# Optimization experiments

Hardware: AMD Instinct MI355X
Metric: run time of the kernel (lower is better)

The kernel has to match this reference:

```python
import jax, jax.numpy as jnp
import numpy as np

B, TD, TE, H, D, V = 64, 256, 256, 512, 256, 50000

def setup_inputs() -> dict:
    key = jax.random.key(0)
    ks = jax.random.split(key, 8)
    return {
        "enc_outputs": jax.random.normal(ks[0], (B, TE, H), jnp.float32),
        "dec_inputs": jax.random.randint(ks[1], (B, TD), 0, V, jnp.int32),
        "state_h": jax.random.normal(ks[2], (B, H), jnp.float32),
        "state_c": jax.random.normal(ks[3], (B, H), jnp.float32),
        "E": jax.random.normal(ks[4], (V, D), jnp.float32) * 0.02,
        "W": jax.random.normal(ks[5], (D, 4 * H), jnp.float32) * 0.02,
        "U": jax.random.normal(ks[6], (H, 4 * H), jnp.float32) * 0.02,
        "b": jnp.zeros((4 * H,), jnp.float32),
    }


def _masked_lstm(x, mask, h0, c0, W, U, b):
    """Keras-semantics masked LSTM: at masked steps states AND outputs are
    carried from the previous step. Gate order i, f, g(cell), o."""
    def step(carry, inp):
        h, c = carry
        xt, mt = inp  # xt: [B,D], mt: [B]
        z = xt @ W + h @ U + b  # [B,4H]
        i, f, g, o = jnp.split(z, 4, axis=-1)
        c_new = jax.nn.sigmoid(f) * c + jax.nn.sigmoid(i) * jnp.tanh(g)
        h_new = jax.nn.sigmoid(o) * jnp.tanh(c_new)
        m = mt[:, None]
        h2 = jnp.where(m, h_new, h)
        c2 = jnp.where(m, c_new, c)
        return (h2, c2), h2
    xs = (jnp.swapaxes(x, 0, 1), jnp.swapaxes(mask, 0, 1))  # time-major
    (hT, cT), hs = jax.lax.scan(step, (h0, c0), xs)
    return jnp.swapaxes(hs, 0, 1), hT, cT  # [B,Td,H]


def reference(enc_outputs, dec_inputs, state_h, state_c, E, W, U, b):
    mask = dec_inputs != 0  # mask_zero=True on Embedding
    x = E[dec_inputs]  # [B,Td,D]
    dec_outputs, hT, cT = _masked_lstm(x, mask, state_h, state_c, W, U, b)
    # Keras Attention (Luong dot, no scale): query=dec_outputs, key=value=enc_outputs
    scores = jnp.einsum('bqh,bkh->bqk', dec_outputs, enc_outputs)
    probs = jax.nn.softmax(scores, axis=-1)
    ctx = jnp.einsum('bqk,bkh->bqh', probs, enc_outputs)
    # query mask propagated from embedding zeroes masked query rows
    ctx = jnp.where(mask[..., None], ctx, 0.0)
    return (ctx, hT, cT)
```

## Files before the change

### kernel.cpp

```cpp
#include <hip/hip_runtime.h>
#include <stdint.h>

typedef __attribute__((ext_vector_type(4))) float f32x4;
typedef __attribute__((ext_vector_type(4))) int i32x4;
typedef __attribute__((ext_vector_type(4))) unsigned short u16x4;
typedef __attribute__((ext_vector_type(8))) __bf16 bf16x8;

#define NB 64
#define TD 256
#define TE 256
#define HH 512
#define DD 256
#define FH 2048
#define KT 768
#define LDK 776

#define WS_ENC   0u
#define WS_ENCT  16777216u
#define WS_DEC   33554432u
#define WS_HPING 50331648u
#define WS_FLAGS 50462720u
#define WS_WT    50528256u

#define OUT_HT 8388608u
#define OUT_CT 8421376u

__device__ inline unsigned short f2b(float f) {
  union { float f; unsigned u; } x; x.f = f;
  unsigned r = x.u + 0x7FFFu + ((x.u >> 16) & 1u);
  return (unsigned short)(r >> 16);
}
__device__ inline float sigm(float x)   { return 1.0f / (1.0f + __expf(-x)); }
__device__ inline float tanhf_(float x) { return 1.0f - 2.0f / (__expf(2.0f * x) + 1.0f); }

__device__ inline f32x4 mfma_bf16(i32x4 a, i32x4 b, f32x4 c) {
  return __builtin_amdgcn_mfma_f32_16x16x32_bf16(
      __builtin_bit_cast(bf16x8, a), __builtin_bit_cast(bf16x8, b), c, 0, 0, 0);
}

__device__ inline unsigned poll_flag(const unsigned* p) {
  unsigned v;
  asm volatile("global_load_dword %0, %1, off sc0 sc1\n\ts_waitcnt vmcnt(0)"
               : "=v"(v) : "v"(p) : "memory");
  return v;
}
__device__ inline void store_u16_wt(unsigned short* p, unsigned v) {
  asm volatile("global_store_short %0, %1, off sc0 sc1" :: "v"(p), "v"(v) : "memory");
}
__device__ inline void store_flag(unsigned* p, unsigned v) {
  asm volatile("s_waitcnt vmcnt(0)\n\tglobal_store_dword %0, %1, off sc0 sc1"
               :: "v"(p), "v"(v) : "memory");
}
__device__ inline void l2_inv() {
  asm volatile("s_waitcnt vmcnt(0)\n\tbuffer_inv sc1" ::: "memory");
}

__global__ __launch_bounds__(256) void enc_prep(const float* __restrict__ enc,
                                                unsigned short* __restrict__ enc_bf,
                                                unsigned short* __restrict__ encT_bf) {
  __shared__ float tile[64][65];
  const int bid = blockIdx.x;
  const int b  = bid >> 5;
  const int kt = (bid >> 3) & 3;
  const int ht = bid & 7;
  const int tr = threadIdx.x >> 6;
  const int tc = threadIdx.x & 63;
#pragma unroll
  for (int i = 0; i < 16; ++i) {
    const int ke = i * 4 + tr;
    const float v = enc[((size_t)b * TE + kt * 64 + ke) * HH + ht * 64 + tc];
    enc_bf[((size_t)b * TE + kt * 64 + ke) * HH + ht * 64 + tc] = f2b(v);
    tile[ke][tc] = v;
  }
  __syncthreads();
  const int hr4 = threadIdx.x >> 4;
  const int k4  = (threadIdx.x & 15) * 4;
#pragma unroll
  for (int jr = 0; jr < 4; ++jr) {
    const int hr = jr * 16 + hr4;
    u16x4 p = { f2b(tile[k4 + 0][hr]), f2b(tile[k4 + 1][hr]),
                f2b(tile[k4 + 2][hr]), f2b(tile[k4 + 3][hr]) };
    *(u16x4*)&encT_bf[((size_t)b * HH + ht * 64 + hr) * TE + kt * 64 + k4] = p;
  }
}

__global__ __launch_bounds__(256) void w_prep(const float* __restrict__ W,
                                              const float* __restrict__ U,
                                              unsigned short* __restrict__ wT) {
  __shared__ float tile[64][65];
  const int kt = blockIdx.x >> 5;
  const int ct = blockIdx.x & 31;
  const int tr = threadIdx.x >> 6;
  const int tc = threadIdx.x & 63;
#pragma unroll
  for (int i = 0; i < 16; ++i) {
    const int kr = i * 4 + tr;
    const int k  = kt * 64 + kr;
    const float v = (k < DD) ? W[(size_t)k * FH + ct * 64 + tc]
                             : U[(size_t)(k - DD) * FH + ct * 64 + tc];
    tile[kr][tc] = v;
  }
  __syncthreads();
  const int cr4 = threadIdx.x >> 4;
  const int k4  = (threadIdx.x & 15) * 4;
#pragma unroll
  for (int jr = 0; jr < 4; ++jr) {
    const int cr = jr * 16 + cr4;
    u16x4 p = { f2b(tile[k4 + 0][cr]), f2b(tile[k4 + 1][cr]),
                f2b(tile[k4 + 2][cr]), f2b(tile[k4 + 3][cr]) };
    *(u16x4*)&wT[((size_t)ct * 64 + cr) * KT + kt * 64 + k4] = p;
  }
}

__global__ __launch_bounds__(256) void h0_prep(const float* __restrict__ h0,
                                               unsigned short* __restrict__ h_ping,
                                               unsigned* __restrict__ flags) {
  const int i = blockIdx.x * 256 + threadIdx.x;
  if (i < NB * HH) h_ping[i] = f2b(h0[i]);
  if (i < 2 * TD * 32) flags[i] = 0u;
}

__global__ __launch_bounds__(64, 1) void lstm_kernel(
    const float* __restrict__ E, const int* __restrict__ ids,
    const float* __restrict__ h0f, const float* __restrict__ c0f,
    const unsigned short* __restrict__ wT, const float* __restrict__ bias,
    unsigned short* __restrict__ h_ping,
    unsigned short* __restrict__ dec_bf,
    float* __restrict__ out,
    unsigned* __restrict__ flags)
{
  const int lane = threadIdx.x;
  const int g  = blockIdx.x >> 5;
  const int s  = blockIdx.x & 31;
  const int u0 = s << 4;
  const int lhi = lane >> 4;
  const int llo = lane & 15;

  __shared__ __align__(16) unsigned short wt[64 * LDK];

  {
    const int r = lane;
    const int c = (r >> 4) * 512 + u0 + (r & 15);
    const unsigned short* src = wT + (size_t)c * KT;
#pragma unroll 8
    for (int j = 0; j < 96; ++j)
      *(i32x4*)&wt[r * LDK + j * 8] = *(const i32x4*)(src + j * 8);
  }
  __syncthreads();

  float bb[4];
#pragma unroll
  for (int gg = 0; gg < 4; ++gg) bb[gg] = bias[gg * 512 + u0 + llo];

  float h_reg[2][4], c_reg[2][4];
#pragma unroll
  for (int mt = 0; mt < 2; ++mt)
#pragma unroll
    for (int r = 0; r < 4; ++r) {
      const int b = g * 32 + mt * 16 + lhi * 4 + r;
      h_reg[mt][r] = h0f[b * HH + u0 + llo];
      c_reg[mt][r] = c0f[b * HH + u0 + llo];
    }

  unsigned short* hp0 = h_ping;
  unsigned short* hp1 = h_ping + NB * HH;

  for (int t = 0; t < TD; ++t) {
    const unsigned short* h_src = (t & 1) ? hp1 : hp0;
    unsigned short*       h_dst = (t & 1) ? hp0 : hp1;

    int xid[2], mid[2][4];
#pragma unroll
    for (int mt = 0; mt < 2; ++mt) {
      xid[mt] = ids[(g * 32 + mt * 16 + llo) * TD + t];
#pragma unroll
      for (int r = 0; r < 4; ++r)
        mid[mt][r] = ids[(g * 32 + mt * 16 + lhi * 4 + r) * TD + t];
    }

    i32x4 xf[2][8];
#pragma unroll
    for (int mt = 0; mt < 2; ++mt)
#pragma unroll
      for (int kk = 0; kk < 8; ++kk) {
        const float* ep = E + (size_t)xid[mt] * DD + kk * 32 + lhi * 8;
        f32x4 lo = *(const f32x4*)ep;
        f32x4 hi = *(const f32x4*)(ep + 4);
        union { i32x4 i; unsigned short sh[8]; } u;
        u.sh[0] = f2b(lo[0]); u.sh[1] = f2b(lo[1]); u.sh[2] = f2b(lo[2]); u.sh[3] = f2b(lo[3]);
        u.sh[4] = f2b(hi[0]); u.sh[5] = f2b(hi[1]); u.sh[6] = f2b(hi[2]); u.sh[7] = f2b(hi[3]);
        xf[mt][kk] = u.i;
      }

    f32x4 acc[2][4];
#pragma unroll
    for (int mt = 0; mt < 2; ++mt)
#pragma unroll
      for (int gg = 0; gg < 4; ++gg) acc[mt][gg] = (f32x4){0.f, 0.f, 0.f, 0.f};
#pragma unroll
    for (int kk = 0; kk < 8; ++kk) {
      const int ko = kk * 32 + lhi * 8;
#pragma unroll
      for (int gg = 0; gg < 4; ++gg) {
        i32x4 bfr = *(const i32x4*)&wt[(gg * 16 + llo) * LDK + ko];
        acc[0][gg] = mfma_bf16(xf[0][kk], bfr, acc[0][gg]);
        acc[1][gg] = mfma_bf16(xf[1][kk], bfr, acc[1][gg]);
      }
    }

    if (t > 0) {
      const unsigned* f = flags + ((size_t)g * TD + (t - 1)) * 32;
      for (;;) {
        unsigned v = (lane < 32) ? poll_flag(f + lane) : 1u;
        if (__all(v != 0)) break;
        __builtin_amdgcn_s_sleep(2);
      }
      l2_inv();
    }

    {
      const unsigned short* hb0 = h_src + (size_t)(g * 32 + llo) * HH + lhi * 8;
      const unsigned short* hb1 = hb0 + 16 * HH;
#pragma unroll
      for (int kk = 0; kk < 16; ++kk) {
        i32x4 a0 = *(const i32x4*)(hb0 + kk * 32);
        i32x4 a1 = *(const i32x4*)(hb1 + kk * 32);
        const int ko = DD + kk * 32 + lhi * 8;
#pragma unroll
        for (int gg = 0; gg < 4; ++gg) {
          i32x4 bfr = *(const i32x4*)&wt[(gg * 16 + llo) * LDK + ko];
          acc[0][gg] = mfma_bf16(a0, bfr, acc[0][gg]);
          acc[1][gg] = mfma_bf16(a1, bfr, acc[1][gg]);
        }
      }
    }

#pragma unroll
    for (int mt = 0; mt < 2; ++mt) {
#pragma unroll
      for (int r = 0; r < 4; ++r) {
        const float zi = acc[mt][0][r] + bb[0];
        const float zf = acc[mt][1][r] + bb[1];
        const float zg = acc[mt][2][r] + bb[2];
        const float zo = acc[mt][3][r] + bb[3];
        const float cn = sigm(zf) * c_reg[mt][r] + sigm(zi) * tanhf_(zg);
        const float hn = sigm(zo) * tanhf_(cn);
        if (mid[mt][r] != 0) { c_reg[mt][r] = cn; h_reg[mt][r] = hn; }
        const int b = g * 32 + mt * 16 + lhi * 4 + r;
        const unsigned hb = f2b(h_reg[mt][r]);
        store_u16_wt(h_dst + (size_t)b * HH + u0 + llo, hb);
        __builtin_nontemporal_store((unsigned short)hb,
            &dec_bf[((size_t)b * TD + t) * HH + u0 + llo]);
      }
    }

    if (t < TD - 1) {
      if (lane == 0)
        store_flag(flags + ((size_t)g * TD + t) * 32 + s, 1u);
      else
        asm volatile("s_waitcnt vmcnt(0)" ::: "memory");
    }
  }

#pragma unroll
  for (int mt = 0; mt < 2; ++mt)
#pragma unroll
    for (int r = 0; r < 4; ++r) {
      const int b = g * 32 + mt * 16 + lhi * 4 + r;
      out[OUT_HT + (size_t)b * HH + u0 + llo] = h_reg[mt][r];
      out[OUT_CT + (size_t)b * HH + u0 + llo] = c_reg[mt][r];
    }
}

__global__ __launch_bounds__(64, 1) void attn_kernel(
    const unsigned short* __restrict__ dec_bf,
    const unsigned short* __restrict__ enc_bf,
    const unsigned short* __restrict__ encT_bf,
    const int* __restrict__ ids,
    float* __restrict__ out)
{
  const int lane = threadIdx.x;
  const int b  = blockIdx.x >> 4;
  const int q0 = (blockIdx.x & 15) << 4;
  const int lhi = lane >> 4, llo = lane & 15;

  __shared__ __align__(16) unsigned short plds[16 * 264];

  i32x4 qf[16];
  const unsigned short* qb = dec_bf + ((size_t)b * TD + q0 + llo) * HH + lhi * 8;
#pragma unroll
  for (int kk = 0; kk < 16; ++kk) qf[kk] = *(const i32x4*)(qb + kk * 32);

  f32x4 sc[16];
#pragma unroll
  for (int ke = 0; ke < 16; ++ke) sc[ke] = (f32x4){0.f, 0.f, 0.f, 0.f};
#pragma unroll
  for (int kk = 0; kk < 16; ++kk) {
    const unsigned short* eb = enc_bf + ((size_t)b * TE + llo) * HH + kk * 32 + lhi * 8;
#pragma unroll
    for (int ke = 0; ke < 16; ++ke)
      sc[ke] = mfma_bf16(qf[kk], *(const i32x4*)(eb + (size_t)ke * 16 * HH), sc[ke]);
  }

  float mx[4], rinv[4];
#pragma unroll
  for (int r = 0; r < 4; ++r) {
    float m = sc[0][r];
#pragma unroll
    for (int ke = 1; ke < 16; ++ke) m = fmaxf(m, sc[ke][r]);
#pragma unroll
    for (int off = 1; off <= 8; off <<= 1) m = fmaxf(m, __shfl_xor(m, off));
    mx[r] = m;
  }
  float sm[4] = {0.f, 0.f, 0.f, 0.f};
#pragma unroll
  for (int ke = 0; ke < 16; ++ke)
#pragma unroll
    for (int r = 0; r < 4; ++r) {
      const float p = __expf(sc[ke][r] - mx[r]);
      sc[ke][r] = p;
      sm[r] += p;
    }
#pragma unroll
  for (int r = 0; r < 4; ++r) {
    float ss = sm[r];
#pragma unroll
    for (int off = 1; off <= 8; off <<= 1) ss += __shfl_xor(ss, off);
    rinv[r] = 1.0f / ss;
  }

#pragma unroll
  for (int ke = 0; ke < 16; ++ke)
#pragma unroll
    for (int r = 0; r < 4; ++r)
      plds[(lhi * 4 + r) * 264 + ke * 16 + llo] = f2b(sc[ke][r]);
  __syncthreads();

  int mq[4];
#pragma unroll
  for (int r = 0; r < 4; ++r) mq[r] = ids[b * TD + q0 + lhi * 4 + r];

  i32x4 pf[8];
#pragma unroll
  for (int k2 = 0; k2 < 8; ++k2)
    pf[k2] = *(const i32x4*)&plds[llo * 264 + k2 * 32 + lhi * 8];

#pragma unroll
  for (int hh = 0; hh < 2; ++hh) {
    f32x4 cacc[16];
#pragma unroll
    for (int hn = 0; hn < 16; ++hn) cacc[hn] = (f32x4){0.f, 0.f, 0.f, 0.f};
#pragma unroll
    for (int k2 = 0; k2 < 8; ++k2) {
      const unsigned short* tb = encT_bf + ((size_t)b * HH + hh * 256 + llo) * TE + k2 * 32 + lhi * 8;
#pragma unroll
      for (int hn = 0; hn < 16; ++hn)
        cacc[hn] = mfma_bf16(pf[k2], *(const i32x4*)(tb + (size_t)hn * 16 * TE), cacc[hn]);
    }
#pragma unroll
    for (int hn = 0; hn < 16; ++hn)
#pragma unroll
      for (int r = 0; r < 4; ++r) {
        const float vv = mq[r] ? cacc[hn][r] * rinv[r] : 0.0f;
        out[((size_t)b * TD + q0 + lhi * 4 + r) * HH + hh * 256 + hn * 16 + llo] = vv;
      }
  }
}

extern "C" void kernel_launch(void* const* d_in, const int* in_sizes, int n_in,
                              void* d_out, int out_size, void* d_ws, size_t ws_size,
                              hipStream_t stream) {
  const float* enc  = (const float*)d_in[0];
  const int*   ids  = (const int*)d_in[1];
  const float* h0   = (const float*)d_in[2];
  const float* c0   = (const float*)d_in[3];
  const float* E    = (const float*)d_in[4];
  const float* W    = (const float*)d_in[5];
  const float* U    = (const float*)d_in[6];
  const float* bias = (const float*)d_in[7];
  float* out = (float*)d_out;
  char* ws = (char*)d_ws;

  unsigned short* enc_bf  = (unsigned short*)(ws + WS_ENC);
  unsigned short* encT_bf = (unsigned short*)(ws + WS_ENCT);
  unsigned short* dec_bf  = (unsigned short*)(ws + WS_DEC);
  unsigned short* h_ping  = (unsigned short*)(ws + WS_HPING);
  unsigned*       flags   = (unsigned*)(ws + WS_FLAGS);
  unsigned short* wT      = (unsigned short*)(ws + WS_WT);

  enc_prep<<<2048, 256, 0, stream>>>(enc, enc_bf, encT_bf);
  w_prep<<<384, 256, 0, stream>>>(W, U, wT);
  h0_prep<<<128, 256, 0, stream>>>(h0, h_ping, flags);
  lstm_kernel<<<64, 64, 0, stream>>>(E, ids, h0, c0, wT, bias, h_ping, dec_bf, out, flags);
  attn_kernel<<<1024, 64, 0, stream>>>(dec_bf, enc_bf, encT_bf, ids, out);
}
```

Measured before the change: 2.253 ms.

## Tighten LSTM step handoff: bypass loads, drop L2 invalidate, stage ids in LDS

The per-step cross-block handoff is restructured. The buffer_inv L2 invalidate is removed, and the h vector is instead read with sc0 sc1 bypass loads, issued as one batch with a single drain before the MFMAs. The h stores and the flag store are now issued before the dec_bf output stores, so the flag waits only on the h stores, and the polling sleep is shortened. Token ids are also preloaded into LDS once per block, so per-step global id loads disappear. The change shortens the serial critical path of the recurrence, but it depends on the bypass loads being coherent without an invalidate and uses more registers and LDS.

```diff
diff --git a/kernel.cpp b/kernel.cpp
--- a/kernel.cpp
+++ b/kernel.cpp
@@ -44,15 +44,19 @@
                : "=v"(v) : "v"(p) : "memory");
   return v;
 }
+__device__ inline i32x4 load4_bypass(const void* p) {
+  i32x4 v;
+  asm volatile("global_load_dwordx4 %0, %1, off sc0 sc1" : "=v"(v) : "v"(p) : "memory");
+  return v;
+}
 __device__ inline void store_u16_wt(unsigned short* p, unsigned v) {
   asm volatile("global_store_short %0, %1, off sc0 sc1" :: "v"(p), "v"(v) : "memory");
 }
+__device__ inline void vm_drain() {
+  asm volatile("s_waitcnt vmcnt(0)" ::: "memory");
+}
 __device__ inline void store_flag(unsigned* p, unsigned v) {
-  asm volatile("s_waitcnt vmcnt(0)\n\tglobal_store_dword %0, %1, off sc0 sc1"
-               :: "v"(p), "v"(v) : "memory");
-}
-__device__ inline void l2_inv() {
-  asm volatile("s_waitcnt vmcnt(0)\n\tbuffer_inv sc1" ::: "memory");
+  asm volatile("global_store_dword %0, %1, off sc0 sc1" :: "v"(p), "v"(v) : "memory");
 }
 
 __global__ __launch_bounds__(256) void enc_prep(const float* __restrict__ enc,
@@ -137,6 +141,7 @@
   const int llo = lane & 15;
 
   __shared__ __align__(16) unsigned short wt[64 * LDK];
+  __shared__ int ids_l[32][260];
 
   {
     const int r = lane;
@@ -146,6 +151,10 @@
     for (int j = 0; j < 96; ++j)
       *(i32x4*)&wt[r * LDK + j * 8] = *(const i32x4*)(src + j * 8);
   }
+  for (int idx = lane; idx < 32 * 256; idx += 64) {
+    const int row = idx >> 8, tt = idx & 255;
+    ids_l[row][tt] = ids[(g * 32 + row) * TD + tt];
+  }
   __syncthreads();
 
   float bb[4];
@@ -172,10 +181,9 @@
     int xid[2], mid[2][4];
 #pragma unroll
     for (int mt = 0; mt < 2; ++mt) {
-      xid[mt] = ids[(g * 32 + mt * 16 + llo) * TD + t];
-#pragma unroll
-      for (int r = 0; r < 4; ++r)
-        mid[mt][r] = ids[(g * 32 + mt * 16 + lhi * 4 + r) * TD + t];
+      xid[mt] = ids_l[mt * 16 + llo][t];
+#pragma unroll
+      for (int r = 0; r < 4; ++r) mid[mt][r] = ids_l[mt * 16 + lhi * 4 + r][t];
     }
 
     i32x4 xf[2][8];
@@ -213,28 +221,34 @@
       for (;;) {
         unsigned v = (lane < 32) ? poll_flag(f + lane) : 1u;
         if (__all(v != 0)) break;
-        __builtin_amdgcn_s_sleep(2);
-      }
-      l2_inv();
+        __builtin_amdgcn_s_sleep(1);
+      }
     }
 
     {
       const unsigned short* hb0 = h_src + (size_t)(g * 32 + llo) * HH + lhi * 8;
       const unsigned short* hb1 = hb0 + 16 * HH;
+      i32x4 ha0[16], ha1[16];
 #pragma unroll
       for (int kk = 0; kk < 16; ++kk) {
-        i32x4 a0 = *(const i32x4*)(hb0 + kk * 32);
-        i32x4 a1 = *(const i32x4*)(hb1 + kk * 32);
+        ha0[kk] = load4_bypass(hb0 + kk * 32);
+        ha1[kk] = load4_bypass(hb1 + kk * 32);
+      }
+      vm_drain();
+      __builtin_amdgcn_sched_barrier(0);
+#pragma unroll
+      for (int kk = 0; kk < 16; ++kk) {
         const int ko = DD + kk * 32 + lhi * 8;
 #pragma unroll
         for (int gg = 0; gg < 4; ++gg) {
           i32x4 bfr = *(const i32x4*)&wt[(gg * 16 + llo) * LDK + ko];
-          acc[0][gg] = mfma_bf16(a0, bfr, acc[0][gg]);
-          acc[1][gg] = mfma_bf16(a1, bfr, acc[1][gg]);
+          acc[0][gg] = mfma_bf16(ha0[kk], bfr, acc[0][gg]);
+          acc[1][gg] = mfma_bf16(ha1[kk], bfr, acc[1][gg]);
         }
       }
     }
 
+    unsigned hb_out[2][4];
 #pragma unroll
     for (int mt = 0; mt < 2; ++mt) {
 #pragma unroll
@@ -246,20 +260,31 @@
         const float cn = sigm(zf) * c_reg[mt][r] + sigm(zi) * tanhf_(zg);
         const float hn = sigm(zo) * tanhf_(cn);
         if (mid[mt][r] != 0) { c_reg[mt][r] = cn; h_reg[mt][r] = hn; }
-        const int b = g * 32 + mt * 16 + lhi * 4 + r;
-        const unsigned hb = f2b(h_reg[mt][r]);
-        store_u16_wt(h_dst + (size_t)b * HH + u0 + llo, hb);
-        __builtin_nontemporal_store((unsigned short)hb,
-            &dec_bf[((size_t)b * TD + t) * HH + u0 + llo]);
+        hb_out[mt][r] = f2b(h_reg[mt][r]);
       }
     }
 
     if (t < TD - 1) {
+#pragma unroll
+      for (int mt = 0; mt < 2; ++mt)
+#pragma unroll
+        for (int r = 0; r < 4; ++r) {
+          const int b = g * 32 + mt * 16 + lhi * 4 + r;
+          store_u16_wt(h_dst + (size_t)b * HH + u0 + llo, hb_out[mt][r]);
+        }
+      vm_drain();
       if (lane == 0)
         store_flag(flags + ((size_t)g * TD + t) * 32 + s, 1u);
-      else
-        asm volatile("s_waitcnt vmcnt(0)" ::: "memory");
-    }
+    }
+
+#pragma unroll
+    for (int mt = 0; mt < 2; ++mt)
+#pragma unroll
+      for (int r = 0; r < 4; ++r) {
+        const int b = g * 32 + mt * 16 + lhi * 4 + r;
+        __builtin_nontemporal_store((unsigned short)hb_out[mt][r],
+            &dec_bf[((size_t)b * TD + t) * HH + u0 + llo]);
+      }
   }
 
 #pragma unroll
```

New measurement: 1.921 ms. 1.17x faster.

## Replace persistent flag-synchronized LSTM kernel with per-timestep kernel launches

Applied to the files above, without the earlier changes.

The persistent LSTM kernel, which used global-memory flags, polling and L2 invalidation to synchronize 64 blocks across timesteps, is replaced by one small kernel launch per timestep. Stream ordering now provides the inter-step barrier. The cell state lives in a global workspace buffer, and the weights are read from global memory (L2) on every step instead of being staged once in LDS. This trades the spin-wait cost for 256 kernel launch overheads plus repeated weight and state traffic. The final hT output now comes from the bf16-rounded h rather than the fp32 register value.

```diff
diff --git a/kernel.cpp b/kernel.cpp
--- a/kernel.cpp
+++ b/kernel.cpp
@@ -13,14 +13,13 @@
 #define DD 256
 #define FH 2048
 #define KT 768
-#define LDK 776
 
 #define WS_ENC   0u
 #define WS_ENCT  16777216u
 #define WS_DEC   33554432u
 #define WS_HPING 50331648u
-#define WS_FLAGS 50462720u
-#define WS_WT    50528256u
+#define WS_CST   50462720u
+#define WS_WT    50593792u
 
 #define OUT_HT 8388608u
 #define OUT_CT 8421376u
@@ -30,29 +29,16 @@
   unsigned r = x.u + 0x7FFFu + ((x.u >> 16) & 1u);
   return (unsigned short)(r >> 16);
 }
+__device__ inline float b2f(unsigned hs) {
+  union { unsigned u; float f; } x; x.u = hs << 16;
+  return x.f;
+}
 __device__ inline float sigm(float x)   { return 1.0f / (1.0f + __expf(-x)); }
 __device__ inline float tanhf_(float x) { return 1.0f - 2.0f / (__expf(2.0f * x) + 1.0f); }
 
 __device__ inline f32x4 mfma_bf16(i32x4 a, i32x4 b, f32x4 c) {
   return __builtin_amdgcn_mfma_f32_16x16x32_bf16(
       __builtin_bit_cast(bf16x8, a), __builtin_bit_cast(bf16x8, b), c, 0, 0, 0);
-}
-
-__device__ inline unsigned poll_flag(const unsigned* p) {
-  unsigned v;
-  asm volatile("global_load_dword %0, %1, off sc0 sc1\n\ts_waitcnt vmcnt(0)"
-               : "=v"(v) : "v"(p) : "memory");
-  return v;
-}
-__device__ inline void store_u16_wt(unsigned short* p, unsigned v) {
-  asm volatile("global_store_short %0, %1, off sc0 sc1" :: "v"(p), "v"(v) : "memory");
-}
-__device__ inline void store_flag(unsigned* p, unsigned v) {
-  asm volatile("s_waitcnt vmcnt(0)\n\tglobal_store_dword %0, %1, off sc0 sc1"
-               :: "v"(p), "v"(v) : "memory");
-}
-__device__ inline void l2_inv() {
-  asm volatile("s_waitcnt vmcnt(0)\n\tbuffer_inv sc1" ::: "memory");
 }
 
 __global__ __launch_bounds__(256) void enc_prep(const float* __restrict__ enc,
@@ -113,21 +99,24 @@
 }
 
 __global__ __launch_bounds__(256) void h0_prep(const float* __restrict__ h0,
+                                               const float* __restrict__ c0,
                                                unsigned short* __restrict__ h_ping,
-                                               unsigned* __restrict__ flags) {
+                                               float* __restrict__ c_st) {
   const int i = blockIdx.x * 256 + threadIdx.x;
-  if (i < NB * HH) h_ping[i] = f2b(h0[i]);
-  if (i < 2 * TD * 32) flags[i] = 0u;
-}
-
-__global__ __launch_bounds__(64, 1) void lstm_kernel(
+  if (i < NB * HH) {
+    h_ping[i] = f2b(h0[i]);
+    c_st[i] = c0[i];
+  }
+}
+
+__global__ __launch_bounds__(64, 1) void lstm_step(
     const float* __restrict__ E, const int* __restrict__ ids,
-    const float* __restrict__ h0f, const float* __restrict__ c0f,
     const unsigned short* __restrict__ wT, const float* __restrict__ bias,
-    unsigned short* __restrict__ h_ping,
+    float* __restrict__ c_st,
+    const unsigned short* __restrict__ h_src,
+    unsigned short* __restrict__ h_dst,
     unsigned short* __restrict__ dec_bf,
-    float* __restrict__ out,
-    unsigned* __restrict__ flags)
+    float* __restrict__ out, int t)
 {
   const int lane = threadIdx.x;
   const int g  = blockIdx.x >> 5;
@@ -136,140 +125,91 @@
   const int lhi = lane >> 4;
   const int llo = lane & 15;
 
-  __shared__ __align__(16) unsigned short wt[64 * LDK];
-
-  {
-    const int r = lane;
-    const int c = (r >> 4) * 512 + u0 + (r & 15);
-    const unsigned short* src = wT + (size_t)c * KT;
-#pragma unroll 8
-    for (int j = 0; j < 96; ++j)
-      *(i32x4*)&wt[r * LDK + j * 8] = *(const i32x4*)(src + j * 8);
-  }
-  __syncthreads();
-
-  float bb[4];
-#pragma unroll
-  for (int gg = 0; gg < 4; ++gg) bb[gg] = bias[gg * 512 + u0 + llo];
-
-  float h_reg[2][4], c_reg[2][4];
+  int xid[2], mid[2][4];
+#pragma unroll
+  for (int mt = 0; mt < 2; ++mt) {
+    xid[mt] = ids[(g * 32 + mt * 16 + llo) * TD + t];
+#pragma unroll
+    for (int r = 0; r < 4; ++r)
+      mid[mt][r] = ids[(g * 32 + mt * 16 + lhi * 4 + r) * TD + t];
+  }
+
+  i32x4 xf[2][8];
 #pragma unroll
   for (int mt = 0; mt < 2; ++mt)
+#pragma unroll
+    for (int kk = 0; kk < 8; ++kk) {
+      const float* ep = E + (size_t)xid[mt] * DD + kk * 32 + lhi * 8;
+      f32x4 lo = *(const f32x4*)ep;
+      f32x4 hi = *(const f32x4*)(ep + 4);
+      union { i32x4 i; unsigned short sh[8]; } u;
+      u.sh[0] = f2b(lo[0]); u.sh[1] = f2b(lo[1]); u.sh[2] = f2b(lo[2]); u.sh[3] = f2b(lo[3]);
+      u.sh[4] = f2b(hi[0]); u.sh[5] = f2b(hi[1]); u.sh[6] = f2b(hi[2]); u.sh[7] = f2b(hi[3]);
+      xf[mt][kk] = u.i;
+    }
+
+  const unsigned short* hb0 = h_src + (size_t)(g * 32 + llo) * HH + lhi * 8;
+  const unsigned short* hb1 = hb0 + 16 * HH;
+  i32x4 ha0[16], ha1[16];
+#pragma unroll
+  for (int kk = 0; kk < 16; ++kk) {
+    ha0[kk] = *(const i32x4*)(hb0 + kk * 32);
+    ha1[kk] = *(const i32x4*)(hb1 + kk * 32);
+  }
+
+  f32x4 acc[2][4];
+#pragma unroll
+  for (int mt = 0; mt < 2; ++mt)
+#pragma unroll
+    for (int gg = 0; gg < 4; ++gg) acc[mt][gg] = (f32x4){0.f, 0.f, 0.f, 0.f};
+
+#pragma unroll
+  for (int kk = 0; kk < 8; ++kk) {
+    const int ko = kk * 32 + lhi * 8;
+#pragma unroll
+    for (int gg = 0; gg < 4; ++gg) {
+      i32x4 bfr = *(const i32x4*)(wT + (size_t)(gg * 512 + u0 + llo) * KT + ko);
+      acc[0][gg] = mfma_bf16(xf[0][kk], bfr, acc[0][gg]);
+      acc[1][gg] = mfma_bf16(xf[1][kk], bfr, acc[1][gg]);
+    }
+  }
+#pragma unroll
+  for (int kk = 0; kk < 16; ++kk) {
+    const int ko = DD + kk * 32 + lhi * 8;
+#pragma unroll
+    for (int gg = 0; gg < 4; ++gg) {
+      i32x4 bfr = *(const i32x4*)(wT + (size_t)(gg * 512 + u0 + llo) * KT + ko);
+      acc[0][gg] = mfma_bf16(ha0[kk], bfr, acc[0][gg]);
+      acc[1][gg] = mfma_bf16(ha1[kk], bfr, acc[1][gg]);
+    }
+  }
+
+#pragma unroll
+  for (int mt = 0; mt < 2; ++mt) {
 #pragma unroll
     for (int r = 0; r < 4; ++r) {
       const int b = g * 32 + mt * 16 + lhi * 4 + r;
-      h_reg[mt][r] = h0f[b * HH + u0 + llo];
-      c_reg[mt][r] = c0f[b * HH + u0 + llo];
-    }
-
-  unsigned short* hp0 = h_ping;
-  unsigned short* hp1 = h_ping + NB * HH;
-
-  for (int t = 0; t < TD; ++t) {
-    const unsigned short* h_src = (t & 1) ? hp1 : hp0;
-    unsigned short*       h_dst = (t & 1) ? hp0 : hp1;
-
-    int xid[2], mid[2][4];
-#pragma unroll
-    for (int mt = 0; mt < 2; ++mt) {
-      xid[mt] = ids[(g * 32 + mt * 16 + llo) * TD + t];
-#pragma unroll
-      for (int r = 0; r < 4; ++r)
-        mid[mt][r] = ids[(g * 32 + mt * 16 + lhi * 4 + r) * TD + t];
-    }
-
-    i32x4 xf[2][8];
-#pragma unroll
-    for (int mt = 0; mt < 2; ++mt)
-#pragma unroll
-      for (int kk = 0; kk < 8; ++kk) {
-        const float* ep = E + (size_t)xid[mt] * DD + kk * 32 + lhi * 8;
-        f32x4 lo = *(const f32x4*)ep;
-        f32x4 hi = *(const f32x4*)(ep + 4);
-        union { i32x4 i; unsigned short sh[8]; } u;
-        u.sh[0] = f2b(lo[0]); u.sh[1] = f2b(lo[1]); u.sh[2] = f2b(lo[2]); u.sh[3] = f2b(lo[3]);
-        u.sh[4] = f2b(hi[0]); u.sh[5] = f2b(hi[1]); u.sh[6] = f2b(hi[2]); u.sh[7] = f2b(hi[3]);
-        xf[mt][kk] = u.i;
+      const size_t si = (size_t)b * HH + u0 + llo;
+      const float zi = acc[mt][0][r] + bias[0 * 512 + u0 + llo];
+      const float zf = acc[mt][1][r] + bias[1 * 512 + u0 + llo];
+      const float zg = acc[mt][2][r] + bias[2 * 512 + u0 + llo];
+      const float zo = acc[mt][3][r] + bias[3 * 512 + u0 + llo];
+      const float c_old = c_st[si];
+      const unsigned h_old = h_src[si];
+      const float cn = sigm(zf) * c_old + sigm(zi) * tanhf_(zg);
+      const float hn = sigm(zo) * tanhf_(cn);
+      const int m = mid[mt][r];
+      const float c_new = m ? cn : c_old;
+      const unsigned hb = m ? f2b(hn) : h_old;
+      c_st[si] = c_new;
+      h_dst[si] = (unsigned short)hb;
+      dec_bf[((size_t)b * TD + t) * HH + u0 + llo] = (unsigned short)hb;
+      if (t == TD - 1) {
+        out[OUT_HT + si] = b2f(hb);
+        out[OUT_CT + si] = c_new;
       }
-
-    f32x4 acc[2][4];
-#pragma unroll
-    for (int mt = 0; mt < 2; ++mt)
-#pragma unroll
-      for (int gg = 0; gg < 4; ++gg) acc[mt][gg] = (f32x4){0.f, 0.f, 0.f, 0.f};
-#pragma unroll
-    for (int kk = 0; kk < 8; ++kk) {
-      const int ko = kk * 32 + lhi * 8;
-#pragma unroll
-      for (int gg = 0; gg < 4; ++gg) {
-        i32x4 bfr = *(const i32x4*)&wt[(gg * 16 + llo) * LDK + ko];
-        acc[0][gg] = mfma_bf16(xf[0][kk], bfr, acc[0][gg]);
-        acc[1][gg] = mfma_bf16(xf[1][kk], bfr, acc[1][gg]);
-      }
-    }
-
-    if (t > 0) {
-      const unsigned* f = flags + ((size_t)g * TD + (t - 1)) * 32;
-      for (;;) {
-        unsigned v = (lane < 32) ? poll_flag(f + lane) : 1u;
-        if (__all(v != 0)) break;
-        __builtin_amdgcn_s_sleep(2);
-      }
-      l2_inv();
-    }
-
-    {
-      const unsigned short* hb0 = h_src + (size_t)(g * 32 + llo) * HH + lhi * 8;
-      const unsigned short* hb1 = hb0 + 16 * HH;
-#pragma unroll
-      for (int kk = 0; kk < 16; ++kk) {
-        i32x4 a0 = *(const i32x4*)(hb0 + kk * 32);
-        i32x4 a1 = *(const i32x4*)(hb1 + kk * 32);
-        const int ko = DD + kk * 32 + lhi * 8;
-#pragma unroll
-        for (int gg = 0; gg < 4; ++gg) {
-          i32x4 bfr = *(const i32x4*)&wt[(gg * 16 + llo) * LDK + ko];
-          acc[0][gg] = mfma_bf16(a0, bfr, acc[0][gg]);
-          acc[1][gg] = mfma_bf16(a1, bfr, acc[1][gg]);
-        }
-      }
-    }
-
-#pragma unroll
-    for (int mt = 0; mt < 2; ++mt) {
-#pragma unroll
-      for (int r = 0; r < 4; ++r) {
-        const float zi = acc[mt][0][r] + bb[0];
-        const float zf = acc[mt][1][r] + bb[1];
-        const float zg = acc[mt][2][r] + bb[2];
-        const float zo = acc[mt][3][r] + bb[3];
-        const float cn = sigm(zf) * c_reg[mt][r] + sigm(zi) * tanhf_(zg);
-        const float hn = sigm(zo) * tanhf_(cn);
-        if (mid[mt][r] != 0) { c_reg[mt][r] = cn; h_reg[mt][r] = hn; }
-        const int b = g * 32 + mt * 16 + lhi * 4 + r;
-        const unsigned hb = f2b(h_reg[mt][r]);
-        store_u16_wt(h_dst + (size_t)b * HH + u0 + llo, hb);
-        __builtin_nontemporal_store((unsigned short)hb,
-            &dec_bf[((size_t)b * TD + t) * HH + u0 + llo]);
-      }
-    }
-
-    if (t < TD - 1) {
-      if (lane == 0)
-        store_flag(flags + ((size_t)g * TD + t) * 32 + s, 1u);
-      else
-        asm volatile("s_waitcnt vmcnt(0)" ::: "memory");
-    }
-  }
-
-#pragma unroll
-  for (int mt = 0; mt < 2; ++mt)
-#pragma unroll
-    for (int r = 0; r < 4; ++r) {
-      const int b = g * 32 + mt * 16 + lhi * 4 + r;
-      out[OUT_HT + (size_t)b * HH + u0 + llo] = h_reg[mt][r];
-      out[OUT_CT + (size_t)b * HH + u0 + llo] = c_reg[mt][r];
-    }
+    }
+  }
 }
 
 __global__ __launch_bounds__(64, 1) void attn_kernel(
@@ -385,12 +325,20 @@
   unsigned short* encT_bf = (unsigned short*)(ws + WS_ENCT);
   unsigned short* dec_bf  = (unsigned short*)(ws + WS_DEC);
   unsigned short* h_ping  = (unsigned short*)(ws + WS_HPING);
-  unsigned*       flags   = (unsigned*)(ws + WS_FLAGS);
+  float*          c_st    = (float*)(ws + WS_CST);
   unsigned short* wT      = (unsigned short*)(ws + WS_WT);
 
   enc_prep<<<2048, 256, 0, stream>>>(enc, enc_bf, encT_bf);
   w_prep<<<384, 256, 0, stream>>>(W, U, wT);
-  h0_prep<<<128, 256, 0, stream>>>(h0, h_ping, flags);
-  lstm_kernel<<<64, 64, 0, stream>>>(E, ids, h0, c0, wT, bias, h_ping, dec_bf, out, flags);
+  h0_prep<<<128, 256, 0, stream>>>(h0, c0, h_ping, c_st);
+
+  unsigned short* hp0 = h_ping;
+  unsigned short* hp1 = h_ping + NB * HH;
+  for (int t = 0; t < TD; ++t) {
+    const unsigned short* hs = (t & 1) ? hp1 : hp0;
+    unsigned short*       hd = (t & 1) ? hp0 : hp1;
+    lstm_step<<<64, 64, 0, stream>>>(E, ids, wT, bias, c_st, hs, hd, dec_bf, out, t);
+  }
+
   attn_kernel<<<1024, 64, 0, stream>>>(dec_bf, enc_bf, encT_bf, ids, out);
 }
```

Result: slower. 4.427 ms (+96.5%).
